# Performance work log

Measured on AMD Instinct MI355X. Metric: run time of the kernel, lower is better.

The kernel has to match this reference:

```python
import jax, jax.numpy as jnp
import numpy as np

BETA = 0.25

def setup_inputs() -> dict:
    key = jax.random.key(0)
    k1, k2 = jax.random.split(key)
    z_e = jax.random.normal(k1, (32768, 256), dtype=jnp.float32)
    codebook = jax.random.normal(k2, (8192, 256), dtype=jnp.float32)
    return {"z_e": z_e, "codebook": codebook}

def reference(z_e, codebook):
    # Squared distances via ||a||^2 - 2 a.b + ||b||^2 (argmin is invariant to sqrt)
    z_sq = jnp.sum(z_e * z_e, axis=1, keepdims=True)           # (B, 1)
    e_sq = jnp.sum(codebook * codebook, axis=1)                 # (K,)
    cross = jnp.einsum('bd,kd->bk', z_e, codebook)              # (B, K) GEMM
    d2 = z_sq - 2.0 * cross + e_sq[None, :]                     # (B, K)
    indices = jnp.argmin(d2, axis=1)                            # (B,)
    z_q = codebook[indices]                                     # (B, D)
    codebook_loss = jnp.mean((z_q - z_e) ** 2)
    commitment_loss = jnp.mean((z_e - z_q) ** 2)
    vq_loss = codebook_loss + BETA * commitment_loss
    # straight-through value (grad semantics irrelevant in fwd-only)
    z_q_st = z_e + (z_q - z_e)
    return (z_q_st, indices, vq_loss)
```

## Files before the change

kernel.cpp:

```cpp
#include <hip/hip_runtime.h>
#include <hip/hip_bf16.h>
#include <stdint.h>

#define M_ROWS 32768
#define N_CODES 8192
#define K_DIM 256
#define NSLICE 32
#define MARGIN 0.25f
#define MAXCAND 2560

#define BM 256
#define BN 256

typedef _Float16 half8 __attribute__((ext_vector_type(8)));
typedef _Float16 h4v __attribute__((ext_vector_type(4)));
typedef float f4v __attribute__((ext_vector_type(4)));
typedef float f32x4 __attribute__((ext_vector_type(4)));
typedef __attribute__((address_space(3))) void lds_void;
typedef const __attribute__((address_space(1))) void gbl_cvoid;

__device__ __forceinline__ unsigned mono32(float f) {
    unsigned u = __float_as_uint(f);
    return (u & 0x80000000u) ? ~u : (u | 0x80000000u);
}
__device__ __forceinline__ unsigned long long pack_key(float d, unsigned col) {
    return ((unsigned long long)mono32(d) << 32) | (unsigned long long)col;
}
__device__ __forceinline__ float unpack_key(unsigned long long k) {
    unsigned m = (unsigned)(k >> 32);
    unsigned u = (m & 0x80000000u) ? (m & 0x7fffffffu) : ~m;
    return __uint_as_float(u);
}
__device__ __forceinline__ void merge2(unsigned long long& b1, unsigned long long& b2,
                                       unsigned long long o1, unsigned long long o2) {
    unsigned long long n1 = b1 < o1 ? b1 : o1;
    unsigned long long hi = b1 < o1 ? o1 : b1;
    unsigned long long l2 = b2 < o2 ? b2 : o2;
    b2 = hi < l2 ? hi : l2;
    b1 = n1;
}

__global__ __launch_bounds__(256) void prep_zh(const float* __restrict__ z,
                                               _Float16* __restrict__ Aq) {
    int e = blockIdx.x * 256 + threadIdx.x;
    int ln = e & 63, kcg = (e >> 6) & 7, R = e >> 9;
    int row = R * 16 + (ln & 15);
    int k = kcg * 32 + (ln >> 4) * 8;
    const f4v* src = (const f4v*)(z + (size_t)row * K_DIM + k);
    f4v v0 = src[0], v1 = src[1];
    half8 h;
    #pragma unroll
    for (int j = 0; j < 4; ++j) h[j] = (_Float16)v0[j];
    #pragma unroll
    for (int j = 0; j < 4; ++j) h[4 + j] = (_Float16)v1[j];
    *(half8*)(Aq + (size_t)e * 8) = h;
}

__global__ __launch_bounds__(256) void prep_bt(const float* __restrict__ cb,
                                               _Float16* __restrict__ Bq) {
    int e = blockIdx.x * 256 + threadIdx.x;
    int ln = e & 63, kcg = (e >> 6) & 7, C = e >> 9;
    int code = C * 16 + (ln & 15);
    int k = kcg * 32 + (ln >> 4) * 8;
    const f4v* src = (const f4v*)(cb + (size_t)code * K_DIM + k);
    f4v v0 = src[0], v1 = src[1];
    half8 h;
    #pragma unroll
    for (int j = 0; j < 4; ++j) h[j] = (_Float16)v0[j];
    #pragma unroll
    for (int j = 0; j < 4; ++j) h[4 + j] = (_Float16)v1[j];
    *(half8*)(Bq + (size_t)e * 8) = h;
}

__global__ __launch_bounds__(256) void prep_esq(const float* __restrict__ cb,
                                                float* __restrict__ esq) {
    int wave = threadIdx.x >> 6, lane = threadIdx.x & 63;
    int row = blockIdx.x * 4 + wave;
    f4v v = *(const f4v*)(cb + (size_t)row * K_DIM + lane * 4);
    float sq = v[0] * v[0] + v[1] * v[1] + v[2] * v[2] + v[3] * v[3];
    #pragma unroll
    for (int m = 32; m; m >>= 1) sq += __shfl_xor(sq, m);
    if (lane == 0) esq[row] = sq;
}

__global__ __launch_bounds__(512) void coarse_gemm(
        const _Float16* __restrict__ Aq, const _Float16* __restrict__ Bq,
        const float* __restrict__ esq, ulonglong2* __restrict__ slices) {
    __shared__ __align__(16) char smem[131072];
    uint2 (*red)[2] = (uint2(*)[2])smem;

    int bid = blockIdx.x;
    int bn = bid & 31;
    int bm = bid >> 5;
    int m0 = bm * BM, n0 = bn * BN;

    int t = threadIdx.x;
    int lane = t & 63, wave = t >> 6;
    int l15 = lane & 15, quad = lane >> 4;
    int wr = wave >> 1, wc = wave & 1;

    float es_adj[8];
    unsigned colb[8];
    #pragma unroll
    for (int ni = 0; ni < 8; ++ni) {
        es_adj[ni] = esq[n0 + wc * 128 + ni * 16 + l15] + 1024.0f;
        colb[ni] = (unsigned)(ni * 16 + l15);
    }

    f32x4 acc[4][8] = {};

    const char* Ab = (const char*)Aq + (size_t)bm * 131072;
    const char* Bb = (const char*)Bq + (size_t)bn * 131072;

    auto stage = [&](int ks, int buf) {
        char* As = smem + buf * 65536;
        char* Bs = As + 32768;
        #pragma unroll
        for (int i = 0; i < 4; ++i) {
            int e = i * 512 + t;
            int RB = e >> 7, kc = (e >> 6) & 1, ln = e & 63;
            size_t goff = ((size_t)(RB * 8 + ks * 2 + kc) << 10) + (size_t)ln * 16;
            __builtin_amdgcn_global_load_lds((gbl_cvoid*)(Ab + goff),
                                             (lds_void*)(As + e * 16), 16, 0, 0);
            __builtin_amdgcn_global_load_lds((gbl_cvoid*)(Bb + goff),
                                             (lds_void*)(Bs + e * 16), 16, 0, 0);
        }
    };

    auto compute = [&](int buf) {
        const char* As = smem + buf * 65536;
        const char* Bs = As + 32768;
        #pragma unroll
        for (int kc = 0; kc < 2; ++kc) {
            half8 a[4], b[8];
            #pragma unroll
            for (int mi = 0; mi < 4; ++mi) {
                int RB = wr * 4 + mi;
                a[mi] = *(const half8*)(As + ((RB * 2 + kc) * 64 + lane) * 16);
            }
            #pragma unroll
            for (int ni = 0; ni < 8; ++ni) {
                int CB = wc * 8 + ni;
                b[ni] = *(const half8*)(Bs + ((CB * 2 + kc) * 64 + lane) * 16);
            }
            #pragma unroll
            for (int mi = 0; mi < 4; ++mi)
                #pragma unroll
                for (int ni = 0; ni < 8; ++ni)
                    acc[mi][ni] = __builtin_amdgcn_mfma_f32_16x16x32_f16(
                        a[mi], b[ni], acc[mi][ni], 0, 0, 0);
        }
    };

    stage(0, 0);
    __syncthreads();
    #pragma unroll
    for (int ks = 0; ks < 4; ++ks) {
        if (ks < 3) stage(ks + 1, (ks + 1) & 1);
        compute(ks & 1);
        __syncthreads();
    }

    #pragma unroll
    for (int mi = 0; mi < 4; ++mi) {
        #pragma unroll
        for (int r = 0; r < 4; ++r) {
            unsigned b1 = 0xFFFFFFFFu, b2 = 0xFFFFFFFFu;
            #pragma unroll
            for (int ni = 0; ni < 8; ++ni) {
                float key = fmaf(-2.0f, acc[mi][ni][r], es_adj[ni]);
                unsigned kb = (__float_as_uint(key) & 0xFFFFFF80u) | colb[ni];
                unsigned hi = kb > b1 ? kb : b1;
                b1 = kb < b1 ? kb : b1;
                b2 = hi < b2 ? hi : b2;
            }
            #pragma unroll
            for (int m = 1; m < 16; m <<= 1) {
                unsigned o1 = (unsigned)__shfl_xor((int)b1, m);
                unsigned o2 = (unsigned)__shfl_xor((int)b2, m);
                unsigned hi = b1 > o1 ? b1 : o1;
                b1 = b1 < o1 ? b1 : o1;
                unsigned l2 = b2 < o2 ? b2 : o2;
                b2 = hi < l2 ? hi : l2;
            }
            if (l15 == 0) {
                int rowl = wr * 64 + mi * 16 + quad * 4 + r;
                red[rowl][wc] = make_uint2(b1, b2);
            }
        }
    }
    __syncthreads();
    if (t < 256) {
        uint2 p0 = red[t][0], p1 = red[t][1];
        unsigned m1 = p0.x < p1.x ? p0.x : p1.x;
        unsigned hi = p0.x < p1.x ? p1.x : p0.x;
        unsigned sel = p1.x < p0.x ? 1u : 0u;
        unsigned l2 = p0.y < p1.y ? p0.y : p1.y;
        unsigned m2 = hi < l2 ? hi : l2;
        unsigned col = (unsigned)n0 + sel * 128u + (m1 & 127u);
        unsigned long long q1 =
            ((unsigned long long)((m1 & 0xFFFFFF80u) | 0x80000000u) << 32) | col;
        unsigned long long q2 =
            ((unsigned long long)((m2 & 0xFFFFFF80u) | 0x80000000u) << 32) |
            0xFFFFFFFFull;
        slices[(size_t)(m0 + t) * NSLICE + bn] = make_ulonglong2(q1, q2);
    }
}

__global__ __launch_bounds__(256) void merge_slices(
        const ulonglong2* __restrict__ slices,
        int* __restrict__ bestidx, int* __restrict__ flags,
        int* __restrict__ list, int* __restrict__ count) {
    int t = threadIdx.x;
    int wave = t >> 6, lane = t & 63;
    int half = lane >> 5, idx = lane & 31;
    int row = blockIdx.x * 8 + wave * 2 + half;
    ulonglong2 p = slices[(size_t)row * NSLICE + idx];
    unsigned long long b1 = p.x, b2 = p.y;
    #pragma unroll
    for (int m = 1; m < 32; m <<= 1) {
        unsigned long long o1 = (unsigned long long)__shfl_xor((long long)b1, m);
        unsigned long long o2 = (unsigned long long)__shfl_xor((long long)b2, m);
        merge2(b1, b2, o1, o2);
    }
    if (idx == 0) {
        bestidx[row] = (int)(unsigned)(b1 & 0xFFFFFFFFULL);
        int f = (unpack_key(b2) - unpack_key(b1) <= MARGIN) ? 1 : 0;
        flags[row] = f;
        if (f) { int pos = atomicAdd(count, 1); list[pos] = row; }
    }
}

__global__ __launch_bounds__(256) void refine(
        const float* __restrict__ z, const float* __restrict__ cb,
        const ulonglong2* __restrict__ slices,
        const int* __restrict__ list, const int* __restrict__ count,
        int* __restrict__ bestidx) {
    __shared__ float zrow[K_DIM];
    __shared__ int cand[MAXCAND];
    __shared__ int ncand_s;
    __shared__ unsigned long long sb1;
    __shared__ double wd[4];
    __shared__ int wc[4];
    int t = threadIdx.x, lane = t & 63, wave = t >> 6;
    int n = *count;
    #pragma unroll 1
    for (int li = blockIdx.x; li < n; li += 2048) {
        int row = list[li];
        __syncthreads();
        zrow[t] = z[(size_t)row * K_DIM + t];
        if (t == 0) ncand_s = 0;
        __syncthreads();
        ulonglong2 p = make_ulonglong2(~0ULL, ~0ULL);
        if (wave == 0) {
            if (lane < NSLICE) p = slices[(size_t)row * NSLICE + lane];
            unsigned long long b1 = p.x;
            #pragma unroll
            for (int m = 1; m < 64; m <<= 1) {
                unsigned long long o =
                    (unsigned long long)__shfl_xor((long long)b1, m);
                b1 = o < b1 ? o : b1;
            }
            if (lane == 0) sb1 = b1;
        }
        __syncthreads();
        float thr = unpack_key(sb1) + MARGIN;
        if (wave == 0 && lane < NSLICE) {
            float k1 = unpack_key(p.x), k2 = unpack_key(p.y);
            if (k2 <= thr) {
                int pos = atomicAdd(&ncand_s, 256);
                if (pos + 256 <= MAXCAND)
                    for (int j = 0; j < 256; ++j) cand[pos + j] = lane * 256 + j;
            } else if (k1 <= thr) {
                int pos = atomicAdd(&ncand_s, 1);
                if (pos < MAXCAND) cand[pos] = (int)(unsigned)(p.x & 0xFFFFFFFFULL);
            }
        }
        __syncthreads();
        int nc = ncand_s;
        bool full = nc > MAXCAND;
        int total = full ? N_CODES : nc;
        double bd = 1e300;
        int bc = 0x7fffffff;
        #pragma unroll 1
        for (int base = 0; base < total; base += 256) {
            int i = base + t;
            if (i < total) {
                int code = full ? i : cand[i];
                const f4v* e4 = (const f4v*)(cb + (size_t)code * K_DIM);
                double s0 = 0, s1 = 0, s2 = 0, s3 = 0;
                #pragma unroll 4
                for (int k4 = 0; k4 < 64; ++k4) {
                    f4v e = e4[k4];
                    f4v zz = *(const f4v*)&zrow[k4 * 4];
                    float d0 = zz[0] - e[0], d1 = zz[1] - e[1];
                    float d2 = zz[2] - e[2], d3 = zz[3] - e[3];
                    s0 = fma((double)d0, (double)d0, s0);
                    s1 = fma((double)d1, (double)d1, s1);
                    s2 = fma((double)d2, (double)d2, s2);
                    s3 = fma((double)d3, (double)d3, s3);
                }
                double s = (s0 + s1) + (s2 + s3);
                if (s < bd || (s == bd && code < bc)) { bd = s; bc = code; }
            }
        }
        #pragma unroll
        for (int m = 1; m < 64; m <<= 1) {
            double od = __shfl_xor(bd, m);
            int oc = __shfl_xor(bc, m);
            if (od < bd || (od == bd && oc < bc)) { bd = od; bc = oc; }
        }
        if (lane == 0) { wd[wave] = bd; wc[wave] = bc; }
        __syncthreads();
        if (t == 0) {
            #pragma unroll
            for (int w = 1; w < 4; ++w)
                if (wd[w] < bd || (wd[w] == bd && wc[w] < bc)) { bd = wd[w]; bc = wc[w]; }
            bestidx[row] = bc;
        }
    }
}

__global__ __launch_bounds__(256) void vq_bruteforce(const float* __restrict__ z,
                                                     const float* __restrict__ cb,
                                                     float* __restrict__ out_idx) {
    __shared__ float As[128 * 16];
    __shared__ float Bs[128 * 16];
    int t = threadIdx.x;
    int tx = t & 15, ty = t >> 4;
    int r0 = blockIdx.x * 128;
    unsigned long long best[8];
    #pragma unroll
    for (int j = 0; j < 8; ++j) best[j] = ~0ULL;

    for (int n0 = 0; n0 < N_CODES; n0 += 128) {
        float acc[8][8] = {};
        for (int k0 = 0; k0 < K_DIM; k0 += 16) {
            __syncthreads();
            int row = t >> 1, c8 = (t & 1) * 8;
            #pragma unroll
            for (int j = 0; j < 8; ++j)
                As[row * 16 + c8 + j] = z[(size_t)(r0 + row) * K_DIM + k0 + c8 + j];
            #pragma unroll
            for (int j = 0; j < 8; ++j)
                Bs[row * 16 + c8 + j] = cb[(size_t)(n0 + row) * K_DIM + k0 + c8 + j];
            __syncthreads();
            #pragma unroll
            for (int k = 0; k < 16; ++k) {
                float a[8], b[8];
                #pragma unroll
                for (int j = 0; j < 8; ++j) a[j] = As[(ty * 8 + j) * 16 + k];
                #pragma unroll
                for (int j = 0; j < 8; ++j) b[j] = Bs[(tx * 8 + j) * 16 + k];
                #pragma unroll
                for (int i = 0; i < 8; ++i)
                    #pragma unroll
                    for (int j = 0; j < 8; ++j) {
                        float d = a[i] - b[j];
                        acc[i][j] += d * d;
                    }
            }
        }
        #pragma unroll
        for (int i = 0; i < 8; ++i) {
            unsigned long long bv = ~0ULL;
            #pragma unroll
            for (int j = 0; j < 8; ++j) {
                unsigned long long p =
                    pack_key(acc[i][j], (unsigned)(n0 + tx * 8 + j));
                bv = (p < bv) ? p : bv;
            }
            #pragma unroll
            for (int m = 1; m < 16; m <<= 1) {
                unsigned long long o =
                    (unsigned long long)__shfl_xor((long long)bv, m);
                bv = (o < bv) ? o : bv;
            }
            if (tx == 0 && bv < best[i]) best[i] = bv;
        }
    }
    if (tx == 0) {
        #pragma unroll
        for (int i = 0; i < 8; ++i)
            out_idx[r0 + ty * 8 + i] =
                (float)(unsigned)(best[i] & 0xFFFFFFFFULL);
    }
}

__global__ __launch_bounds__(256) void finalize(const float* __restrict__ z,
                                                const float* __restrict__ cb,
                                                const int* __restrict__ bestidx,
                                                float* __restrict__ out,
                                                double* __restrict__ accum,
                                                int use_int) {
    int wave = threadIdx.x >> 6, lane = threadIdx.x & 63;
    float* out_idx = out + (size_t)M_ROWS * K_DIM;
    float se = 0.f;
    #pragma unroll 1
    for (int row = blockIdx.x * 4 + wave; row < M_ROWS; row += 1024 * 4) {
        int idx = use_int ? bestidx[row] : (int)out_idx[row];
        f4v zv = *(const f4v*)(z  + (size_t)row * K_DIM + lane * 4);
        f4v qv = *(const f4v*)(cb + (size_t)idx * K_DIM + lane * 4);
        f4v ov;
        #pragma unroll
        for (int j = 0; j < 4; ++j) {
            float d = qv[j] - zv[j];
            ov[j] = zv[j] + d;
            se += d * d;
        }
        *(f4v*)(out + (size_t)row * K_DIM + lane * 4) = ov;
        if (lane == 0) out_idx[row] = (float)idx;
    }
    #pragma unroll
    for (int m = 32; m; m >>= 1) se += __shfl_xor(se, m);
    __shared__ float part[4];
    if (lane == 0) part[wave] = se;
    __syncthreads();
    if (threadIdx.x == 0)
        atomicAdd(accum, (double)((part[0] + part[1]) + (part[2] + part[3])));
}

__global__ void write_loss(const double* __restrict__ accum,
                           float* __restrict__ out) {
    out[(size_t)M_ROWS * K_DIM + M_ROWS] =
        (float)(1.25 * (*accum / (double)((size_t)M_ROWS * K_DIM)));
}

extern "C" void kernel_launch(void* const* d_in, const int* in_sizes, int n_in,
                              void* d_out, int out_size, void* d_ws, size_t ws_size,
                              hipStream_t stream) {
    const float* z  = (const float*)d_in[0];
    const float* cb = (const float*)d_in[1];
    float* out = (float*)d_out;
    float* out_idx = out + (size_t)M_ROWS * K_DIM;

    size_t offA  = 0;
    size_t offBq = offA + (size_t)M_ROWS * K_DIM * 2;
    size_t offE  = offBq + (size_t)N_CODES * K_DIM * 2;
    size_t offS  = offE + (size_t)N_CODES * 4;
    size_t offBI = offS + (size_t)M_ROWS * NSLICE * 16;
    size_t offF  = offBI + (size_t)M_ROWS * 4;
    size_t offL  = offF + (size_t)M_ROWS * 4;
    size_t offC  = offL + (size_t)M_ROWS * 4;
    size_t offAcc = offC + 16;
    size_t need  = offAcc + 16;

    if (ws_size >= need) {
        _Float16* Aq = (_Float16*)((char*)d_ws + offA);
        _Float16* Bq = (_Float16*)((char*)d_ws + offBq);
        float* esq   = (float*)((char*)d_ws + offE);
        ulonglong2* slices = (ulonglong2*)((char*)d_ws + offS);
        int* bestidx = (int*)((char*)d_ws + offBI);
        int* flags   = (int*)((char*)d_ws + offF);
        int* list    = (int*)((char*)d_ws + offL);
        int* count   = (int*)((char*)d_ws + offC);
        double* accum = (double*)((char*)d_ws + offAcc);

        hipMemsetAsync((char*)d_ws + offC, 0, 32, stream);

        prep_zh<<<(M_ROWS / 16) * 8 * 64 / 256, 256, 0, stream>>>(z, Aq);
        prep_bt<<<(N_CODES / 16) * 8 * 64 / 256, 256, 0, stream>>>(cb, Bq);
        prep_esq<<<N_CODES / 4, 256, 0, stream>>>(cb, esq);
        coarse_gemm<<<(M_ROWS / BM) * (N_CODES / BN), 512, 0, stream>>>(
            Aq, Bq, esq, slices);
        merge_slices<<<M_ROWS / 8, 256, 0, stream>>>(slices, bestidx, flags,
                                                     list, count);
        refine<<<2048, 256, 0, stream>>>(z, cb, slices, list, count, bestidx);
        finalize<<<1024, 256, 0, stream>>>(z, cb, bestidx, out, accum, 1);
        write_loss<<<1, 1, 0, stream>>>(accum, out);
    } else {
        double* accum = (double*)d_ws;
        hipMemsetAsync(d_ws, 0, sizeof(double), stream);
        vq_bruteforce<<<M_ROWS / 128, 256, 0, stream>>>(z, cb, out_idx);
        finalize<<<1024, 256, 0, stream>>>(z, cb, nullptr, out, accum, 0);
        write_loss<<<1, 1, 0, stream>>>(accum, out);
    }
}
```

Baseline: 332.1 us.

## Software-pipeline LDS fragment loads against MFMAs in coarse GEMM

The four-step K loop of the coarse GEMM is unrolled by hand into a schedule that double-buffers the A/B fragments in registers. Loading one K-chunk's fragments from LDS now overlaps the MFMAs on the previous chunk. Both global stages are issued up front, and partial vmcnt waits replace full syncthreads. The MFMA blocks are wrapped in s_setprio, and the esq loads are moved to after the main loop. The launch bound now asks for two blocks per CU, which tightens the register budget and risks spills, even though 128 KB of LDS per block may allow only one block to be resident.

```diff
diff --git a/kernel.cpp b/kernel.cpp
--- a/kernel.cpp
+++ b/kernel.cpp
@@ -83,7 +83,7 @@
     if (lane == 0) esq[row] = sq;
 }
 
-__global__ __launch_bounds__(512) void coarse_gemm(
+__global__ __launch_bounds__(512, 2) void coarse_gemm(
         const _Float16* __restrict__ Aq, const _Float16* __restrict__ Bq,
         const float* __restrict__ esq, ulonglong2* __restrict__ slices) {
     __shared__ __align__(16) char smem[131072];
@@ -99,15 +99,8 @@
     int l15 = lane & 15, quad = lane >> 4;
     int wr = wave >> 1, wc = wave & 1;
 
-    float es_adj[8];
-    unsigned colb[8];
-    #pragma unroll
-    for (int ni = 0; ni < 8; ++ni) {
-        es_adj[ni] = esq[n0 + wc * 128 + ni * 16 + l15] + 1024.0f;
-        colb[ni] = (unsigned)(ni * 16 + l15);
-    }
-
     f32x4 acc[4][8] = {};
+    half8 aF[2][4], bF[2][8];
 
     const char* Ab = (const char*)Aq + (size_t)bm * 131072;
     const char* Bb = (const char*)Bq + (size_t)bn * 131072;
@@ -127,39 +120,69 @@
         }
     };
 
-    auto compute = [&](int buf) {
+    auto prefetch = [&](int buf, int kc, int p) {
         const char* As = smem + buf * 65536;
         const char* Bs = As + 32768;
         #pragma unroll
-        for (int kc = 0; kc < 2; ++kc) {
-            half8 a[4], b[8];
-            #pragma unroll
-            for (int mi = 0; mi < 4; ++mi) {
-                int RB = wr * 4 + mi;
-                a[mi] = *(const half8*)(As + ((RB * 2 + kc) * 64 + lane) * 16);
-            }
-            #pragma unroll
-            for (int ni = 0; ni < 8; ++ni) {
-                int CB = wc * 8 + ni;
-                b[ni] = *(const half8*)(Bs + ((CB * 2 + kc) * 64 + lane) * 16);
-            }
-            #pragma unroll
-            for (int mi = 0; mi < 4; ++mi)
-                #pragma unroll
-                for (int ni = 0; ni < 8; ++ni)
-                    acc[mi][ni] = __builtin_amdgcn_mfma_f32_16x16x32_f16(
-                        a[mi], b[ni], acc[mi][ni], 0, 0, 0);
-        }
+        for (int mi = 0; mi < 4; ++mi)
+            aF[p][mi] = *(const half8*)(As +
+                (((wr * 4 + mi) * 2 + kc) * 64 + lane) * 16);
+        #pragma unroll
+        for (int ni = 0; ni < 8; ++ni)
+            bF[p][ni] = *(const half8*)(Bs +
+                (((wc * 8 + ni) * 2 + kc) * 64 + lane) * 16);
     };
+    auto mma = [&](int p) {
+        __builtin_amdgcn_s_setprio(1);
+        #pragma unroll
+        for (int mi = 0; mi < 4; ++mi)
+            #pragma unroll
+            for (int ni = 0; ni < 8; ++ni)
+                acc[mi][ni] = __builtin_amdgcn_mfma_f32_16x16x32_f16(
+                    aF[p][mi], bF[p][ni], acc[mi][ni], 0, 0, 0);
+        __builtin_amdgcn_s_setprio(0);
+    };
 
     stage(0, 0);
-    __syncthreads();
-    #pragma unroll
-    for (int ks = 0; ks < 4; ++ks) {
-        if (ks < 3) stage(ks + 1, (ks + 1) & 1);
-        compute(ks & 1);
-        __syncthreads();
-    }
+    stage(1, 1);
+    asm volatile("s_waitcnt vmcnt(8)" ::: "memory");
+    __builtin_amdgcn_s_barrier();
+    asm volatile("" ::: "memory");
+
+    prefetch(0, 0, 0);
+    prefetch(0, 1, 1);
+    mma(0);
+    asm volatile("s_waitcnt vmcnt(0) lgkmcnt(0)" ::: "memory");
+    __builtin_amdgcn_s_barrier();
+    asm volatile("" ::: "memory");
+    stage(2, 0);
+    prefetch(1, 0, 0);
+    mma(1);
+    prefetch(1, 1, 1);
+    mma(0);
+    asm volatile("s_waitcnt vmcnt(0) lgkmcnt(0)" ::: "memory");
+    __builtin_amdgcn_s_barrier();
+    asm volatile("" ::: "memory");
+    stage(3, 1);
+    prefetch(0, 0, 0);
+    mma(1);
+    prefetch(0, 1, 1);
+    mma(0);
+    asm volatile("s_waitcnt vmcnt(0) lgkmcnt(0)" ::: "memory");
+    __builtin_amdgcn_s_barrier();
+    asm volatile("" ::: "memory");
+    float es_adj[8];
+    unsigned colb[8];
+    #pragma unroll
+    for (int ni = 0; ni < 8; ++ni) {
+        es_adj[ni] = esq[n0 + wc * 128 + ni * 16 + l15] + 1024.0f;
+        colb[ni] = (unsigned)(ni * 16 + l15);
+    }
+    prefetch(1, 0, 0);
+    mma(1);
+    prefetch(1, 1, 1);
+    mma(0);
+    mma(1);
 
     #pragma unroll
     for (int mi = 0; mi < 4; ++mi) {
```

After: 352.6 us. 6.2% more time.

## Deepen coarse GEMM pipeline to four k-stages and fuse prep kernels

Applied to the files above, without the earlier changes.

The coarse GEMM now stages 32-wide k chunks into a 4-deep LDS ring with explicit vmcnt waits and one barrier per step, replacing the 2-buffer 64-wide scheme with a full __syncthreads after each compute. Loads for step ks+2 are issued after fragments for step ks are read into registers, and setprio raises wave priority around the MFMA block. Launch bounds ask for two 512-thread blocks per CU, and the colb array is dropped. The three prep kernels are merged into one launch to save launch overhead. The risks are register pressure under the occupancy hint and hand-written waitcnt correctness.

```diff
diff --git a/kernel.cpp b/kernel.cpp
--- a/kernel.cpp
+++ b/kernel.cpp
@@ -13,7 +13,6 @@
 #define BN 256
 
 typedef _Float16 half8 __attribute__((ext_vector_type(8)));
-typedef _Float16 h4v __attribute__((ext_vector_type(4)));
 typedef float f4v __attribute__((ext_vector_type(4)));
 typedef float f32x4 __attribute__((ext_vector_type(4)));
 typedef __attribute__((address_space(3))) void lds_void;
@@ -40,50 +39,39 @@
     b1 = n1;
 }
 
-__global__ __launch_bounds__(256) void prep_zh(const float* __restrict__ z,
-                                               _Float16* __restrict__ Aq) {
-    int e = blockIdx.x * 256 + threadIdx.x;
-    int ln = e & 63, kcg = (e >> 6) & 7, R = e >> 9;
-    int row = R * 16 + (ln & 15);
-    int k = kcg * 32 + (ln >> 4) * 8;
-    const f4v* src = (const f4v*)(z + (size_t)row * K_DIM + k);
-    f4v v0 = src[0], v1 = src[1];
-    half8 h;
-    #pragma unroll
-    for (int j = 0; j < 4; ++j) h[j] = (_Float16)v0[j];
-    #pragma unroll
-    for (int j = 0; j < 4; ++j) h[4 + j] = (_Float16)v1[j];
-    *(half8*)(Aq + (size_t)e * 8) = h;
-}
-
-__global__ __launch_bounds__(256) void prep_bt(const float* __restrict__ cb,
-                                               _Float16* __restrict__ Bq) {
-    int e = blockIdx.x * 256 + threadIdx.x;
-    int ln = e & 63, kcg = (e >> 6) & 7, C = e >> 9;
-    int code = C * 16 + (ln & 15);
-    int k = kcg * 32 + (ln >> 4) * 8;
-    const f4v* src = (const f4v*)(cb + (size_t)code * K_DIM + k);
-    f4v v0 = src[0], v1 = src[1];
-    half8 h;
-    #pragma unroll
-    for (int j = 0; j < 4; ++j) h[j] = (_Float16)v0[j];
-    #pragma unroll
-    for (int j = 0; j < 4; ++j) h[4 + j] = (_Float16)v1[j];
-    *(half8*)(Bq + (size_t)e * 8) = h;
-}
-
-__global__ __launch_bounds__(256) void prep_esq(const float* __restrict__ cb,
+__global__ __launch_bounds__(256) void prep_all(const float* __restrict__ z,
+                                                const float* __restrict__ cb,
+                                                _Float16* __restrict__ Aq,
+                                                _Float16* __restrict__ Bq,
                                                 float* __restrict__ esq) {
-    int wave = threadIdx.x >> 6, lane = threadIdx.x & 63;
-    int row = blockIdx.x * 4 + wave;
-    f4v v = *(const f4v*)(cb + (size_t)row * K_DIM + lane * 4);
-    float sq = v[0] * v[0] + v[1] * v[1] + v[2] * v[2] + v[3] * v[3];
-    #pragma unroll
-    for (int m = 32; m; m >>= 1) sq += __shfl_xor(sq, m);
-    if (lane == 0) esq[row] = sq;
-}
-
-__global__ __launch_bounds__(512) void coarse_gemm(
+    int b = blockIdx.x;
+    if (b < 5120) {
+        const float* src = (b < 4096) ? z : cb;
+        _Float16* dst = (b < 4096) ? Aq : Bq;
+        int e = (b < 4096 ? b : b - 4096) * 256 + threadIdx.x;
+        int ln = e & 63, kcg = (e >> 6) & 7, R = e >> 9;
+        int row = R * 16 + (ln & 15);
+        int k = kcg * 32 + (ln >> 4) * 8;
+        const f4v* s4 = (const f4v*)(src + (size_t)row * K_DIM + k);
+        f4v v0 = s4[0], v1 = s4[1];
+        half8 h;
+        #pragma unroll
+        for (int j = 0; j < 4; ++j) h[j] = (_Float16)v0[j];
+        #pragma unroll
+        for (int j = 0; j < 4; ++j) h[4 + j] = (_Float16)v1[j];
+        *(half8*)(dst + (size_t)e * 8) = h;
+    } else {
+        int wave = threadIdx.x >> 6, lane = threadIdx.x & 63;
+        int row = (b - 5120) * 4 + wave;
+        f4v v = *(const f4v*)(cb + (size_t)row * K_DIM + lane * 4);
+        float sq = v[0] * v[0] + v[1] * v[1] + v[2] * v[2] + v[3] * v[3];
+        #pragma unroll
+        for (int m = 32; m; m >>= 1) sq += __shfl_xor(sq, m);
+        if (lane == 0) esq[row] = sq;
+    }
+}
+
+__global__ __launch_bounds__(512, 2) void coarse_gemm(
         const _Float16* __restrict__ Aq, const _Float16* __restrict__ Bq,
         const float* __restrict__ esq, ulonglong2* __restrict__ slices) {
     __shared__ __align__(16) char smem[131072];
@@ -100,12 +88,10 @@
     int wr = wave >> 1, wc = wave & 1;
 
     float es_adj[8];
-    unsigned colb[8];
     #pragma unroll
-    for (int ni = 0; ni < 8; ++ni) {
+    for (int ni = 0; ni < 8; ++ni)
         es_adj[ni] = esq[n0 + wc * 128 + ni * 16 + l15] + 1024.0f;
-        colb[ni] = (unsigned)(ni * 16 + l15);
-    }
+    asm volatile("" ::: "memory");
 
     f32x4 acc[4][8] = {};
 
@@ -113,13 +99,13 @@
     const char* Bb = (const char*)Bq + (size_t)bn * 131072;
 
     auto stage = [&](int ks, int buf) {
-        char* As = smem + buf * 65536;
-        char* Bs = As + 32768;
-        #pragma unroll
-        for (int i = 0; i < 4; ++i) {
+        char* As = smem + buf * 32768;
+        char* Bs = As + 16384;
+        #pragma unroll
+        for (int i = 0; i < 2; ++i) {
             int e = i * 512 + t;
-            int RB = e >> 7, kc = (e >> 6) & 1, ln = e & 63;
-            size_t goff = ((size_t)(RB * 8 + ks * 2 + kc) << 10) + (size_t)ln * 16;
+            int RB = e >> 6, ln = e & 63;
+            size_t goff = ((size_t)(RB * 8 + ks) << 10) + (size_t)ln * 16;
             __builtin_amdgcn_global_load_lds((gbl_cvoid*)(Ab + goff),
                                              (lds_void*)(As + e * 16), 16, 0, 0);
             __builtin_amdgcn_global_load_lds((gbl_cvoid*)(Bb + goff),
@@ -127,39 +113,40 @@
         }
     };
 
-    auto compute = [&](int buf) {
-        const char* As = smem + buf * 65536;
-        const char* Bs = As + 32768;
-        #pragma unroll
-        for (int kc = 0; kc < 2; ++kc) {
-            half8 a[4], b[8];
-            #pragma unroll
-            for (int mi = 0; mi < 4; ++mi) {
-                int RB = wr * 4 + mi;
-                a[mi] = *(const half8*)(As + ((RB * 2 + kc) * 64 + lane) * 16);
-            }
-            #pragma unroll
-            for (int ni = 0; ni < 8; ++ni) {
-                int CB = wc * 8 + ni;
-                b[ni] = *(const half8*)(Bs + ((CB * 2 + kc) * 64 + lane) * 16);
-            }
-            #pragma unroll
-            for (int mi = 0; mi < 4; ++mi)
-                #pragma unroll
-                for (int ni = 0; ni < 8; ++ni)
-                    acc[mi][ni] = __builtin_amdgcn_mfma_f32_16x16x32_f16(
-                        a[mi], b[ni], acc[mi][ni], 0, 0, 0);
-        }
+    stage(0, 0);
+    stage(1, 1);
+
+    half8 a[4], b[8];
+    auto body = [&](int ks, bool do_stage) {
+        __builtin_amdgcn_s_barrier();
+        asm volatile("" ::: "memory");
+        const char* As = smem + (ks & 3) * 32768;
+        const char* Bs = As + 16384;
+        #pragma unroll
+        for (int mi = 0; mi < 4; ++mi)
+            a[mi] = *(const half8*)(As + ((wr * 4 + mi) * 64 + lane) * 16);
+        #pragma unroll
+        for (int ni = 0; ni < 8; ++ni)
+            b[ni] = *(const half8*)(Bs + ((wc * 8 + ni) * 64 + lane) * 16);
+        if (do_stage) stage(ks + 2, (ks + 2) & 3);
+        __builtin_amdgcn_s_setprio(1);
+        #pragma unroll
+        for (int mi = 0; mi < 4; ++mi)
+            #pragma unroll
+            for (int ni = 0; ni < 8; ++ni)
+                acc[mi][ni] = __builtin_amdgcn_mfma_f32_16x16x32_f16(
+                    a[mi], b[ni], acc[mi][ni], 0, 0, 0);
+        __builtin_amdgcn_s_setprio(0);
     };
 
-    stage(0, 0);
-    __syncthreads();
-    #pragma unroll
-    for (int ks = 0; ks < 4; ++ks) {
-        if (ks < 3) stage(ks + 1, (ks + 1) & 1);
-        compute(ks & 1);
-        __syncthreads();
-    }
+    asm volatile("s_waitcnt vmcnt(4)" ::: "memory"); body(0, true);
+    asm volatile("s_waitcnt vmcnt(4)" ::: "memory"); body(1, true);
+    asm volatile("s_waitcnt vmcnt(4)" ::: "memory"); body(2, true);
+    asm volatile("s_waitcnt vmcnt(4)" ::: "memory"); body(3, true);
+    asm volatile("s_waitcnt vmcnt(4)" ::: "memory"); body(4, true);
+    asm volatile("s_waitcnt vmcnt(4)" ::: "memory"); body(5, true);
+    asm volatile("s_waitcnt vmcnt(4)" ::: "memory"); body(6, false);
+    asm volatile("s_waitcnt vmcnt(0)" ::: "memory"); body(7, false);
 
     #pragma unroll
     for (int mi = 0; mi < 4; ++mi) {
@@ -169,7 +156,8 @@
             #pragma unroll
             for (int ni = 0; ni < 8; ++ni) {
                 float key = fmaf(-2.0f, acc[mi][ni][r], es_adj[ni]);
-                unsigned kb = (__float_as_uint(key) & 0xFFFFFF80u) | colb[ni];
+                unsigned kb = (__float_as_uint(key) & 0xFFFFFF80u) |
+                              (unsigned)(ni * 16 + l15);
                 unsigned hi = kb > b1 ? kb : b1;
                 b1 = kb < b1 ? kb : b1;
                 b2 = hi < b2 ? hi : b2;
@@ -458,9 +446,7 @@
 
         hipMemsetAsync((char*)d_ws + offC, 0, 32, stream);
 
-        prep_zh<<<(M_ROWS / 16) * 8 * 64 / 256, 256, 0, stream>>>(z, Aq);
-        prep_bt<<<(N_CODES / 16) * 8 * 64 / 256, 256, 0, stream>>>(cb, Bq);
-        prep_esq<<<N_CODES / 4, 256, 0, stream>>>(cb, esq);
+        prep_all<<<7168, 256, 0, stream>>>(z, cb, Aq, Bq, esq);
         coarse_gemm<<<(M_ROWS / BM) * (N_CODES / BN), 512, 0, stream>>>(
             Aq, Bq, esq, slices);
         merge_slices<<<M_ROWS / 8, 256, 0, stream>>>(slices, bestidx, flags,
```

New measurement: 342.2 us. 3.0% more time.
